# Kernel optimization log

Measured on AMD Instinct MI355X. Metric: run time of the kernel, lower is better.

## Reference

```python
import jax, jax.numpy as jnp
import numpy as np

B, S_SRC, S_TGT = 4096, 32, 32
V_SRC, V_TGT, E, H = 96, 128, 128, 512
SOS = 1


def _lstm_cell(h, c, x, Wih, Whh, bih, bhh):
    # PyTorch LSTM gate layout: [i, f, g, o] along 4H
    gates = x @ Wih.T + bih + h @ Whh.T + bhh  # (B, 4H)
    i, f, g, o = jnp.split(gates, 4, axis=-1)
    i, f, o = jax.nn.sigmoid(i), jax.nn.sigmoid(f), jax.nn.sigmoid(o)
    g = jnp.tanh(g)
    c2 = f * c + i * g
    h2 = o * jnp.tanh(c2)
    return h2, c2


def setup_inputs() -> dict:
    key = jax.random.key(0)
    ks = jax.random.split(key, 16)
    u = lambda k, shp, s: jax.random.uniform(k, shp, jnp.float32, -s, s)
    sh = 1.0 / np.sqrt(H)
    emb_src = u(ks[0], (V_SRC, E), 0.1).at[0].set(0.0)  # padding_idx=0
    emb_tgt = u(ks[1], (V_TGT, E), 0.1).at[0].set(0.0)
    inp = {
        "src_seq": jax.random.randint(ks[2], (B, S_SRC), 1, V_SRC),
        "src_lengths": jax.random.randint(ks[3], (B,), 1, S_SRC + 1),
        "tgt_seq": jax.random.randint(ks[4], (B, S_TGT), 1, V_TGT),
        "emb_src": emb_src,
        "enc_Wih": u(ks[5], (4 * H, E), sh),
        "enc_Whh": u(ks[6], (4 * H, H), sh),
        "enc_bih": u(ks[7], (4 * H,), sh),
        "enc_bhh": u(ks[8], (4 * H,), sh),
        "emb_tgt": emb_tgt,
        "dec_Wih": u(ks[9], (4 * H, E), sh),
        "dec_Whh": u(ks[10], (4 * H, H), sh),
        "dec_bih": u(ks[11], (4 * H,), sh),
        "dec_bhh": u(ks[12], (4 * H,), sh),
        "W_out": u(ks[13], (V_TGT, H), sh),
        "b_out": u(ks[14], (V_TGT,), sh),
    }
    return inp


def reference(src_seq, src_lengths, tgt_seq,
              emb_src, enc_Wih, enc_Whh, enc_bih, enc_bhh,
              emb_tgt, dec_Wih, dec_Whh, dec_bih, dec_bhh,
              W_out, b_out):
    batch = src_seq.shape[0]
    h0 = jnp.zeros((batch, H), jnp.float32)
    c0 = jnp.zeros((batch, H), jnp.float32)

    # ---- Encoder: masked LSTM == pack_padded_sequence semantics ----
    x_src = emb_src[src_seq]                                # (B, S, E)
    x_src_t = jnp.swapaxes(x_src, 0, 1)                     # (S, B, E)
    mask = (jnp.arange(S_SRC)[:, None] < src_lengths[None, :])[:, :, None]  # (S,B,1)

    def enc_step(carry, inp):
        h, c = carry
        x, m = inp
        h2, c2 = _lstm_cell(h, c, x, enc_Wih, enc_Whh, enc_bih, enc_bhh)
        h = jnp.where(m, h2, h)
        c = jnp.where(m, c2, c)
        return (h, c), None

    (h_enc, c_enc), _ = jax.lax.scan(enc_step, (h0, c0), (x_src_t, mask))

    # ---- Decoder: full teacher forcing (ratio=1.0), eval-mode dropout ----
    dec_in = jnp.concatenate(
        [jnp.full((batch, 1), SOS, tgt_seq.dtype), tgt_seq[:, :-1]], axis=1)  # (B, T)
    x_tgt_t = jnp.swapaxes(emb_tgt[dec_in], 0, 1)           # (T, B, E)

    def dec_step(carry, x):
        h, c = carry
        h2, c2 = _lstm_cell(h, c, x, dec_Wih, dec_Whh, dec_bih, dec_bhh)
        return (h2, c2), h2

    _, hs = jax.lax.scan(dec_step, (h_enc, c_enc), x_tgt_t)  # (T, B, H)

    logits = jnp.einsum('tbh,vh->btv', hs, W_out) + b_out    # (B, T, V_TGT)
    return logits
```

## Files before the change

kernel.cpp:

```cpp
#include <hip/hip_runtime.h>
#include <hip/hip_bf16.h>
#include <hip/hip_fp16.h>
#include <stdint.h>


#define NB     4096
#define SSRC   32
#define STGT   32
#define NVSRC  96
#define NVTGT  128
#define ED     128
#define HD     512
#define G4     2048
#define NBHD   ((size_t)NB * HD)

typedef __attribute__((ext_vector_type(8))) _Float16 half8;
typedef __attribute__((ext_vector_type(4))) float fx4;

#define AS_G __attribute__((address_space(1)))
#define AS_L __attribute__((address_space(3)))

__device__ __forceinline__ void gl2lds16(const void* g, void* l) {
    __builtin_amdgcn_global_load_lds((const AS_G uint32_t*)g, (AS_L uint32_t*)l, 16, 0, 0);
}

__device__ __forceinline__ float sigf(float x) { return 1.0f / (1.0f + __expf(-x)); }
__device__ __forceinline__ float tanhfast(float x) { return 1.0f - 2.0f / (__expf(2.0f * x) + 1.0f); }

__global__ __launch_bounds__(256) void convert_all(
    const float* __restrict__ s1, int n1, _Float16* __restrict__ d1,
    const float* __restrict__ s2, int n2, _Float16* __restrict__ d2,
    const float* __restrict__ s3, int n3, _Float16* __restrict__ d3)
{
    int i = (int)blockIdx.x * 256 + threadIdx.x;
    if (i < n1) { d1[i] = (_Float16)s1[i]; return; }
    i -= n1;
    if (i < n2) { d2[i] = (_Float16)s2[i]; return; }
    i -= n2;
    if (i < n3) d3[i] = (_Float16)s3[i];
}

__global__ __launch_bounds__(256) void transpose_f32(
    const float* __restrict__ in, float* __restrict__ outT, int R, int C, int rtiles)
{
    __shared__ float ls[32][33];
    const int bx = (int)blockIdx.x % rtiles;
    const int by = (int)blockIdx.x / rtiles;
    const int tx = threadIdx.x & 31, ty = threadIdx.x >> 5;
    #pragma unroll
    for (int i = 0; i < 4; i++) {
        int rr = ty + i * 8;
        ls[rr][tx] = in[(size_t)(bx * 32 + rr) * C + by * 32 + tx];
    }
    __syncthreads();
    #pragma unroll
    for (int i = 0; i < 4; i++) {
        int rr = ty + i * 8;
        outT[(size_t)(by * 32 + rr) * R + bx * 32 + tx] = ls[tx][rr];
    }
}

__global__ __launch_bounds__(256) void build_tables3(
    const float* __restrict__ emb, const float* __restrict__ WT,
    const float* __restrict__ bih, const float* __restrict__ bhh,
    float* __restrict__ proj)
{
    __shared__ float embL[8][ED];
    const int gc = (int)blockIdx.x & 7;
    const int vc = (int)blockIdx.x >> 3;
    const int g  = gc * 256 + threadIdx.x;
    for (int i = threadIdx.x; i < 8 * ED; i += 256)
        embL[i >> 7][i & (ED - 1)] = emb[(size_t)(vc * 8 + (i >> 7)) * ED + (i & (ED - 1))];
    __syncthreads();
    float acc[8] = {0, 0, 0, 0, 0, 0, 0, 0};
    for (int e = 0; e < ED; e++) {
        float w = WT[(size_t)e * G4 + g];
        #pragma unroll
        for (int v = 0; v < 8; v++) acc[v] += embL[v][e] * w;
    }
    float bb = bih[g] + bhh[g];
    const int gate = g >> 9, hcol = g & (HD - 1);
    #pragma unroll
    for (int v = 0; v < 8; v++)
        proj[(((size_t)(vc * 8 + v) * HD + hcol) << 2) + gate] = acc[v] + bb;
}

__global__ __launch_bounds__(256) void sort_rows(
    const int* __restrict__ lens, int* __restrict__ perm,
    int* __restrict__ lens_s, int* __restrict__ maxlen)
{
    __shared__ int hist[33];
    __shared__ int base[33];
    const int tid = threadIdx.x;
    if (tid < 33) hist[tid] = 0;
    __syncthreads();
    for (int i = tid; i < NB; i += 256) atomicAdd(&hist[lens[i]], 1);
    __syncthreads();
    if (tid == 0) {
        int s = 0;
        for (int l = 1; l <= 32; l++) { base[l] = s; s += hist[l]; }
    }
    __syncthreads();
    for (int i = tid; i < NB; i += 256) {
        int l = lens[i];
        int pos = atomicAdd(&base[l], 1);
        perm[pos] = i;
        lens_s[pos] = l;
    }
    __syncthreads();
    if (tid < 32) maxlen[tid] = lens_s[tid * 128 + 127];
}

__global__ __launch_bounds__(256) void gather_seq2(
    const int* __restrict__ src, const int* __restrict__ tgt,
    const int* __restrict__ perm,
    int* __restrict__ src_s, int* __restrict__ tgt_s)
{
    int i = (int)blockIdx.x * 256 + threadIdx.x;
    int half = i >> 17;
    int k = i & ((NB * 32) - 1);
    int row = k >> 5, t = k & 31;
    if (half == 0) src_s[k] = src[perm[row] * 32 + t];
    else           tgt_s[k] = tgt[perm[row] * 32 + t];
}

__global__ __launch_bounds__(512, 4) void lstm_step(
    const _Float16* __restrict__ h_r, _Float16* __restrict__ h_w,
    float* __restrict__ c_state,
    const float* __restrict__ proj,
    const int* __restrict__ seq_s, const int* __restrict__ lens_s,
    const int* __restrict__ maxlen,
    const _Float16* __restrict__ W,
    _Float16* __restrict__ hfinal,
    int t, int is_enc, int skip_gemm)
{
    __shared__ __align__(16) _Float16 lsA[128 * 64];
    __shared__ __align__(16) _Float16 lsB[128 * 64];

    const int tid = threadIdx.x;
    const int lane = tid & 63;
    const int wid  = tid >> 6;
    const int srow = lane >> 3;
    const int skc  = (((lane & 7) ^ srow)) << 3;
    const int wm   = (wid & 3) * 32;
    const int hgrp = (wid >> 2) * 16;
    const int quad = lane >> 4;
    const int l15  = lane & 15;

    const int x = (int)blockIdx.x & 7, j = (int)blockIdx.x >> 3;
    const int mt = (x & 1) * 16 + (j & 15);
    const int m0 = mt * 128;
    const int c0 = ((x >> 1) * 4 + (j >> 4)) * 32;

    if (is_enc && t >= maxlen[mt]) return;

    const _Float16 *ag[2], *bg[2];
    #pragma unroll
    for (int i = 0; i < 2; i++) {
        int lr = wid * 16 + i * 8 + srow;
        ag[i] = h_r + (size_t)(m0 + lr) * HD + skc;
        int wr = (lr >> 5) * HD + c0 + (lr & 31);
        bg[i] = W + (size_t)wr * HD + skc;
    }

    fx4 acc[2][4];
    #pragma unroll
    for (int i = 0; i < 2; i++)
        #pragma unroll
        for (int jj = 0; jj < 4; jj++)
            acc[i][jj] = fx4{0.f, 0.f, 0.f, 0.f};

    if (!skip_gemm) {
        for (int k0 = 0; k0 < HD; k0 += 64) {
            __syncthreads();
            #pragma unroll
            for (int i = 0; i < 2; i++) {
                gl2lds16(ag[i] + k0, &lsA[(wid * 16 + i * 8) * 64]);
                gl2lds16(bg[i] + k0, &lsB[(wid * 16 + i * 8) * 64]);
            }
            __syncthreads();
            #pragma unroll
            for (int kk = 0; kk < 64; kk += 32) {
                const int kc = (kk >> 3) + quad;
                half8 af[2], bf[4];
                #pragma unroll
                for (int mf = 0; mf < 2; mf++) {
                    int ar = wm + mf * 16 + l15;
                    int sw = ((kc ^ (ar & 7)) << 3);
                    af[mf] = *(const half8*)&lsA[ar * 64 + sw];
                }
                #pragma unroll
                for (int g = 0; g < 4; g++) {
                    int br = g * 32 + hgrp + l15;
                    int sw = ((kc ^ (br & 7)) << 3);
                    bf[g] = *(const half8*)&lsB[br * 64 + sw];
                }
                #pragma unroll
                for (int mf = 0; mf < 2; mf++)
                    #pragma unroll
                    for (int g = 0; g < 4; g++)
                        acc[mf][g] = __builtin_amdgcn_mfma_f32_16x16x32_f16(af[mf], bf[g], acc[mf][g], 0, 0, 0);
            }
        }
    }

    const int hcol = c0 + hgrp + l15;
    #pragma unroll
    for (int mf = 0; mf < 2; mf++) {
        #pragma unroll
        for (int r = 0; r < 4; r++) {
            int row = m0 + wm + mf * 16 + quad * 4 + r;
            int tok = is_enc ? seq_s[row * SSRC + t]
                             : (t == 0 ? 1 : seq_s[row * STGT + t - 1]);
            const fx4 xp = *(const fx4*)&proj[((size_t)tok * HD + hcol) << 2];
            float gi = acc[mf][0][r] + xp[0];
            float gf = acc[mf][1][r] + xp[1];
            float gg = acc[mf][2][r] + xp[2];
            float go = acc[mf][3][r] + xp[3];
            float ii = sigf(gi), ff = sigf(gf), oo = sigf(go);
            float g2 = tanhfast(gg);
            size_t off = (size_t)row * HD + hcol;
            float cold = c_state[off];
            float c2 = ff * cold + ii * g2;
            float h2 = oo * tanhfast(c2);
            bool cwrite = true;
            if (is_enc) {
                int len = lens_s[row];
                if (t >= len) {
                    c2 = cold;
                    cwrite = false;
                    h2 = (float)h_r[off];
                }
                if (t + 1 == len)
                    hfinal[off] = (_Float16)h2;
            }
            if (cwrite) c_state[off] = c2;
            h_w[off] = (_Float16)h2;
        }
    }
}

__global__ __launch_bounds__(256, 2) void outproj_batch(
    const _Float16* __restrict__ h_slots, int t0,
    const _Float16* __restrict__ Wo, const float* __restrict__ bout,
    const int* __restrict__ perm,
    float* __restrict__ out)
{
    __shared__ __align__(16) _Float16 lsA[128 * 64];
    __shared__ __align__(16) _Float16 lsB[128 * 64];

    const int tid = threadIdx.x;
    const int lane = tid & 63;
    const int wid  = tid >> 6;
    const int srow = lane >> 3;
    const int skc  = (((lane & 7) ^ srow)) << 3;
    const int wm    = (wid >> 1) * 64;
    const int wncol = wid & 1;
    const int quad  = lane >> 4;
    const int l15   = lane & 15;
    const int bsw   = (l15 & 7);

    const int t  = t0 + ((int)blockIdx.x >> 5);
    const int m0 = ((int)blockIdx.x & 31) * 128;
    const _Float16* h_r = h_slots + (size_t)(t & 15) * NBHD;

    const _Float16 *ag[4], *bg[4];
    #pragma unroll
    for (int i = 0; i < 4; i++) {
        int lr = wid * 32 + i * 8 + srow;
        ag[i] = h_r + (size_t)(m0 + lr) * HD + skc;
        bg[i] = Wo + (size_t)lr * HD + skc;
    }

    fx4 acc[4][4];
    #pragma unroll
    for (int i = 0; i < 4; i++)
        #pragma unroll
        for (int jj = 0; jj < 4; jj++)
            acc[i][jj] = fx4{0.f, 0.f, 0.f, 0.f};

    for (int k0 = 0; k0 < HD; k0 += 64) {
        __syncthreads();
        #pragma unroll
        for (int i = 0; i < 4; i++) {
            int lb = (wid * 32 + i * 8) * 64;
            gl2lds16(ag[i] + k0, &lsA[lb]);
            gl2lds16(bg[i] + k0, &lsB[lb]);
        }
        __syncthreads();
        #pragma unroll
        for (int kk = 0; kk < 64; kk += 32) {
            const int kc = (kk >> 3) + quad;
            const int sw = ((kc ^ bsw) << 3);
            half8 af[4], bf[4];
            #pragma unroll
            for (int mt = 0; mt < 4; mt++)
                af[mt] = *(const half8*)&lsA[(wm + mt * 16 + l15) * 64 + sw];
            #pragma unroll
            for (int nt = 0; nt < 4; nt++)
                bf[nt] = *(const half8*)&lsB[(wncol * 64 + nt * 16 + l15) * 64 + sw];
            #pragma unroll
            for (int mt = 0; mt < 4; mt++)
                #pragma unroll
                for (int nt = 0; nt < 4; nt++)
                    acc[mt][nt] = __builtin_amdgcn_mfma_f32_16x16x32_f16(af[mt], bf[nt], acc[mt][nt], 0, 0, 0);
        }
    }

    #pragma unroll
    for (int mt = 0; mt < 4; mt++)
        #pragma unroll
        for (int nt = 0; nt < 4; nt++) {
            int v = wncol * 64 + nt * 16 + l15;
            float bo = bout[v];
            #pragma unroll
            for (int r = 0; r < 4; r++) {
                int row = m0 + wm + mt * 16 + quad * 4 + r;
                int orow = perm[row];
                out[((size_t)orow * STGT + t) * NVTGT + v] = acc[mt][nt][r] + bo;
            }
        }
}

extern "C" void kernel_launch(void* const* d_in, const int* in_sizes, int n_in,
                              void* d_out, int out_size, void* d_ws, size_t ws_size,
                              hipStream_t stream) {
    (void)in_sizes; (void)n_in; (void)out_size; (void)ws_size;
    const int* src_seq = (const int*)d_in[0];
    const int* src_len = (const int*)d_in[1];
    const int* tgt_seq = (const int*)d_in[2];
    const float* emb_src = (const float*)d_in[3];
    const float* eWih = (const float*)d_in[4];
    const float* eWhh = (const float*)d_in[5];
    const float* ebih = (const float*)d_in[6];
    const float* ebhh = (const float*)d_in[7];
    const float* emb_tgt = (const float*)d_in[8];
    const float* dWih = (const float*)d_in[9];
    const float* dWhh = (const float*)d_in[10];
    const float* dbih = (const float*)d_in[11];
    const float* dbhh = (const float*)d_in[12];
    const float* Wout = (const float*)d_in[13];
    const float* bout = (const float*)d_in[14];
    float* out = (float*)d_out;

    char* ws = (char*)d_ws;
    size_t off = 0;
    auto carve = [&](size_t bytes) { void* p = ws + off; off += (bytes + 255) & ~(size_t)255; return p; };
    float* proj_src = (float*)carve((size_t)NVSRC * G4 * 4);
    float* proj_tgt = (float*)carve((size_t)NVTGT * G4 * 4);
    float* c_state  = (float*)carve(NBHD * 4);
    _Float16* slots = (_Float16*)carve((size_t)18 * NBHD * 2);
    _Float16* eW_h  = (_Float16*)carve((size_t)G4 * HD * 2);
    _Float16* dW_h  = (_Float16*)carve((size_t)G4 * HD * 2);
    _Float16* Wo_h  = (_Float16*)carve((size_t)NVTGT * HD * 2);
    _Float16* hfinal = (_Float16*)carve(NBHD * 2);
    int* perm   = (int*)carve((size_t)NB * 4);
    int* lens_s = (int*)carve((size_t)NB * 4);
    int* maxlen = (int*)carve(32 * 4);
    int* src_s  = (int*)carve((size_t)NB * SSRC * 4);
    int* tgt_s  = (int*)carve((size_t)NB * STGT * 4);
    float* WT_e = (float*)(slots);
    float* WT_d = (float*)((char*)slots + (size_t)ED * G4 * 4);
    auto slot = [&](int i) { return slots + (size_t)i * NBHD; };

    hipMemsetAsync(c_state, 0, NBHD * 4, stream);

    sort_rows<<<dim3(1), dim3(256), 0, stream>>>(src_len, perm, lens_s, maxlen);
    gather_seq2<<<dim3(2 * NB * SSRC / 256), dim3(256), 0, stream>>>(
        src_seq, tgt_seq, perm, src_s, tgt_s);

    {
        int n1 = G4 * HD, n2 = G4 * HD, n3 = NVTGT * HD;
        int nb = (n1 + n2 + n3 + 255) / 256;
        convert_all<<<dim3(nb), dim3(256), 0, stream>>>(
            eWhh, n1, eW_h, dWhh, n2, dW_h, Wout, n3, Wo_h);
    }
    transpose_f32<<<dim3((G4 / 32) * (ED / 32)), dim3(256), 0, stream>>>(eWih, WT_e, G4, ED, G4 / 32);
    transpose_f32<<<dim3((G4 / 32) * (ED / 32)), dim3(256), 0, stream>>>(dWih, WT_d, G4, ED, G4 / 32);
    build_tables3<<<dim3((NVSRC / 8) * 8), dim3(256), 0, stream>>>(emb_src, WT_e, ebih, ebhh, proj_src);
    build_tables3<<<dim3((NVTGT / 8) * 8), dim3(256), 0, stream>>>(emb_tgt, WT_d, dbih, dbhh, proj_tgt);

    for (int s = 0; s < 32; s++) {
        lstm_step<<<dim3(512), dim3(512), 0, stream>>>(
            slot(16 + (s & 1)), slot(16 + ((s + 1) & 1)), c_state,
            proj_src, src_s, lens_s, maxlen, eW_h, hfinal, s, 1, (s == 0));
    }
    for (int t = 0; t < 32; t++) {
        const _Float16* hr = (t == 0) ? hfinal : slot((t - 1) & 15);
        lstm_step<<<dim3(512), dim3(512), 0, stream>>>(
            hr, slot(t & 15), c_state,
            proj_tgt, tgt_s, lens_s, maxlen, dW_h, hfinal, t, 0, 0);
        if ((t & 15) == 15) {
            outproj_batch<<<dim3(512), dim3(256), 0, stream>>>(
                slots, t - 15, Wo_h, bout, perm, out);
        }
    }
}
```

Measured before the change: 1.370 ms.

## Fuse output projection into next decoder LSTM step reusing loaded hidden tiles

The decoder step kernel now also computes logits for the previous timestep, reusing the hidden-state tiles it already loads into LDS. Even column-tile blocks load a 16-row slice of W_out and issue an extra MFMA per k-chunk. Only the last timestep is handled by a small separate launch. The setup transpose and table-building kernels are each merged into a single launch. This adds register/LDS pressure and imbalance between blocks.

Result: no change. 1.374 ms (+0.3%).

```diff
diff --git a/kernel.cpp b/kernel.cpp
--- a/kernel.cpp
+++ b/kernel.cpp
@@ -40,34 +40,47 @@
     if (i < n3) d3[i] = (_Float16)s3[i];
 }
 
-__global__ __launch_bounds__(256) void transpose_f32(
-    const float* __restrict__ in, float* __restrict__ outT, int R, int C, int rtiles)
+__global__ __launch_bounds__(256) void transpose2_f32(
+    const float* __restrict__ inA, float* __restrict__ outTA,
+    const float* __restrict__ inB, float* __restrict__ outTB)
 {
     __shared__ float ls[32][33];
-    const int bx = (int)blockIdx.x % rtiles;
-    const int by = (int)blockIdx.x / rtiles;
+    int bid = (int)blockIdx.x;
+    const float* in; float* outT;
+    if (bid < 256) { in = inA; outT = outTA; }
+    else           { in = inB; outT = outTB; bid -= 256; }
+    const int rtiles = G4 / 32;
+    const int bx = bid % rtiles;
+    const int by = bid / rtiles;
     const int tx = threadIdx.x & 31, ty = threadIdx.x >> 5;
     #pragma unroll
     for (int i = 0; i < 4; i++) {
         int rr = ty + i * 8;
-        ls[rr][tx] = in[(size_t)(bx * 32 + rr) * C + by * 32 + tx];
+        ls[rr][tx] = in[(size_t)(bx * 32 + rr) * ED + by * 32 + tx];
     }
     __syncthreads();
     #pragma unroll
     for (int i = 0; i < 4; i++) {
         int rr = ty + i * 8;
-        outT[(size_t)(by * 32 + rr) * R + bx * 32 + tx] = ls[tx][rr];
-    }
-}
-
-__global__ __launch_bounds__(256) void build_tables3(
-    const float* __restrict__ emb, const float* __restrict__ WT,
-    const float* __restrict__ bih, const float* __restrict__ bhh,
-    float* __restrict__ proj)
+        outT[(size_t)(by * 32 + rr) * G4 + bx * 32 + tx] = ls[tx][rr];
+    }
+}
+
+__global__ __launch_bounds__(256) void build_tables2(
+    const float* __restrict__ embS, const float* __restrict__ WTS,
+    const float* __restrict__ bihS, const float* __restrict__ bhhS,
+    float* __restrict__ projS,
+    const float* __restrict__ embT, const float* __restrict__ WTT,
+    const float* __restrict__ bihT, const float* __restrict__ bhhT,
+    float* __restrict__ projT)
 {
     __shared__ float embL[8][ED];
-    const int gc = (int)blockIdx.x & 7;
-    const int vc = (int)blockIdx.x >> 3;
+    int bid = (int)blockIdx.x;
+    const float *emb, *WT, *bih, *bhh; float* proj;
+    if (bid < (NVSRC / 8) * 8) { emb = embS; WT = WTS; bih = bihS; bhh = bhhS; proj = projS; }
+    else { bid -= (NVSRC / 8) * 8; emb = embT; WT = WTT; bih = bihT; bhh = bhhT; proj = projT; }
+    const int gc = bid & 7;
+    const int vc = bid >> 3;
     const int g  = gc * 256 + threadIdx.x;
     for (int i = threadIdx.x; i < 8 * ED; i += 256)
         embL[i >> 7][i & (ED - 1)] = emb[(size_t)(vc * 8 + (i >> 7)) * ED + (i & (ED - 1))];
@@ -132,10 +145,13 @@
     const int* __restrict__ maxlen,
     const _Float16* __restrict__ W,
     _Float16* __restrict__ hfinal,
+    const _Float16* __restrict__ Wo, const float* __restrict__ bout,
+    const int* __restrict__ perm, float* __restrict__ out,
     int t, int is_enc, int skip_gemm)
 {
     __shared__ __align__(16) _Float16 lsA[128 * 64];
     __shared__ __align__(16) _Float16 lsB[128 * 64];
+    __shared__ __align__(16) _Float16 lsBo[16 * 64];
 
     const int tid = threadIdx.x;
     const int lane = tid & 63;
@@ -150,9 +166,13 @@
     const int x = (int)blockIdx.x & 7, j = (int)blockIdx.x >> 3;
     const int mt = (x & 1) * 16 + (j & 15);
     const int m0 = mt * 128;
-    const int c0 = ((x >> 1) * 4 + (j >> 4)) * 32;
+    const int ct = (x >> 1) * 4 + (j >> 4);
+    const int c0 = ct * 32;
 
     if (is_enc && t >= maxlen[mt]) return;
+
+    const bool po = (!is_enc) && (t > 0) && ((ct & 1) == 0);
+    const int vg = ct >> 1;
 
     const _Float16 *ag[2], *bg[2];
     #pragma unroll
@@ -162,6 +182,7 @@
         int wr = (lr >> 5) * HD + c0 + (lr & 31);
         bg[i] = W + (size_t)wr * HD + skc;
     }
+    const _Float16* bo = Wo + (size_t)(vg * 16 + wid * 8 + srow) * HD + skc;
 
     fx4 acc[2][4];
     #pragma unroll
@@ -169,6 +190,7 @@
         #pragma unroll
         for (int jj = 0; jj < 4; jj++)
             acc[i][jj] = fx4{0.f, 0.f, 0.f, 0.f};
+    fx4 acc_o = fx4{0.f, 0.f, 0.f, 0.f};
 
     if (!skip_gemm) {
         for (int k0 = 0; k0 < HD; k0 += 64) {
@@ -178,6 +200,8 @@
                 gl2lds16(ag[i] + k0, &lsA[(wid * 16 + i * 8) * 64]);
                 gl2lds16(bg[i] + k0, &lsB[(wid * 16 + i * 8) * 64]);
             }
+            if (po && wid < 2)
+                gl2lds16(bo + k0, &lsBo[(wid * 8) * 64]);
             __syncthreads();
             #pragma unroll
             for (int kk = 0; kk < 64; kk += 32) {
@@ -200,6 +224,11 @@
                     #pragma unroll
                     for (int g = 0; g < 4; g++)
                         acc[mf][g] = __builtin_amdgcn_mfma_f32_16x16x32_f16(af[mf], bf[g], acc[mf][g], 0, 0, 0);
+                if (po) {
+                    half8 afo = (wid >> 2) ? af[1] : af[0];
+                    half8 bfo = *(const half8*)&lsBo[l15 * 64 + ((kc ^ (l15 & 7)) << 3)];
+                    acc_o = __builtin_amdgcn_mfma_f32_16x16x32_f16(afo, bfo, acc_o, 0, 0, 0);
+                }
             }
         }
     }
@@ -238,6 +267,18 @@
             h_w[off] = (_Float16)h2;
         }
     }
+
+    if (po) {
+        const int mfo = wid >> 2;
+        const int v = vg * 16 + l15;
+        const float bo_b = bout[v];
+        #pragma unroll
+        for (int r = 0; r < 4; r++) {
+            int row = m0 + wm + mfo * 16 + quad * 4 + r;
+            int orow = perm[row];
+            out[((size_t)orow * STGT + (t - 1)) * NVTGT + v] = acc_o[r] + bo_b;
+        }
+    }
 }
 
 __global__ __launch_bounds__(256, 2) void outproj_batch(
@@ -375,24 +416,24 @@
         convert_all<<<dim3(nb), dim3(256), 0, stream>>>(
             eWhh, n1, eW_h, dWhh, n2, dW_h, Wout, n3, Wo_h);
     }
-    transpose_f32<<<dim3((G4 / 32) * (ED / 32)), dim3(256), 0, stream>>>(eWih, WT_e, G4, ED, G4 / 32);
-    transpose_f32<<<dim3((G4 / 32) * (ED / 32)), dim3(256), 0, stream>>>(dWih, WT_d, G4, ED, G4 / 32);
-    build_tables3<<<dim3((NVSRC / 8) * 8), dim3(256), 0, stream>>>(emb_src, WT_e, ebih, ebhh, proj_src);
-    build_tables3<<<dim3((NVTGT / 8) * 8), dim3(256), 0, stream>>>(emb_tgt, WT_d, dbih, dbhh, proj_tgt);
+    transpose2_f32<<<dim3(512), dim3(256), 0, stream>>>(eWih, WT_e, dWih, WT_d);
+    build_tables2<<<dim3((NVSRC / 8) * 8 + (NVTGT / 8) * 8), dim3(256), 0, stream>>>(
+        emb_src, WT_e, ebih, ebhh, proj_src,
+        emb_tgt, WT_d, dbih, dbhh, proj_tgt);
 
     for (int s = 0; s < 32; s++) {
         lstm_step<<<dim3(512), dim3(512), 0, stream>>>(
             slot(16 + (s & 1)), slot(16 + ((s + 1) & 1)), c_state,
-            proj_src, src_s, lens_s, maxlen, eW_h, hfinal, s, 1, (s == 0));
+            proj_src, src_s, lens_s, maxlen, eW_h, hfinal,
+            Wo_h, bout, perm, out, s, 1, (s == 0));
     }
     for (int t = 0; t < 32; t++) {
         const _Float16* hr = (t == 0) ? hfinal : slot((t - 1) & 15);
         lstm_step<<<dim3(512), dim3(512), 0, stream>>>(
             hr, slot(t & 15), c_state,
-            proj_tgt, tgt_s, lens_s, maxlen, dW_h, hfinal, t, 0, 0);
-        if ((t & 15) == 15) {
-            outproj_batch<<<dim3(512), dim3(256), 0, stream>>>(
-                slots, t - 15, Wo_h, bout, perm, out);
-        }
-    }
-}
+            proj_tgt, tgt_s, lens_s, maxlen, dW_h, hfinal,
+            Wo_h, bout, perm, out, t, 0, 0);
+    }
+    outproj_batch<<<dim3(32), dim3(256), 0, stream>>>(
+        slots, 31, Wo_h, bout, perm, out);
+}
```
